# Performance work log

Hardware: AMD Instinct MI355X
Metric: run time of the kernel (lower is better)

## Reference

```python
import jax, jax.numpy as jnp
import numpy as np

B = 16
DRUG_LEN, PROT_LEN = 64, 1200
DIM, CONV = 64, 40


def conv1d(x, w, b):
    # x: [B, C_in, L], w: [C_out, C_in, K] (torch layout), VALID padding
    y = jax.lax.conv_general_dilated(
        x, w, window_strides=(1,), padding='VALID',
        dimension_numbers=('NCH', 'OIH', 'NCH'))
    return y + b[None, :, None]


def setup_inputs() -> dict:
    key = jax.random.key(0)
    ks = jax.random.split(key, 32)
    s = 0.05
    inp = {
        'drug_tokens': jax.random.randint(ks[0], (B, DRUG_LEN), 0, 65, dtype=jnp.int32),
        'protein_tokens': jax.random.randint(ks[1], (B, PROT_LEN), 0, 26, dtype=jnp.int32),
        'drug_emb': (jax.random.normal(ks[2], (65, DIM)) * s).at[0].set(0.0),
        'prot_emb': (jax.random.normal(ks[3], (26, DIM)) * s).at[0].set(0.0),
        'dW1': jax.random.normal(ks[4], (CONV, DIM, 4)) * s,
        'db1': jax.random.normal(ks[5], (CONV,)) * s,
        'dW2': jax.random.normal(ks[6], (CONV * 2, CONV, 6)) * s,
        'db2': jax.random.normal(ks[7], (CONV * 2,)) * s,
        'dW3': jax.random.normal(ks[8], (CONV * 4, CONV * 2, 8)) * s,
        'db3': jax.random.normal(ks[9], (CONV * 4,)) * s,
        'pW1': jax.random.normal(ks[10], (CONV, DIM, 4)) * s,
        'pb1': jax.random.normal(ks[11], (CONV,)) * s,
        'pW2': jax.random.normal(ks[12], (CONV * 2, CONV, 8)) * s,
        'pb2': jax.random.normal(ks[13], (CONV * 2,)) * s,
        'pW3': jax.random.normal(ks[14], (CONV * 4, CONV * 2, 12)) * s,
        'pb3': jax.random.normal(ks[15], (CONV * 4,)) * s,
        'dattW': jax.random.normal(ks[16], (160, 160)) * s,
        'dattb': jax.random.normal(ks[17], (160,)) * s,
        'pattW': jax.random.normal(ks[18], (160, 160)) * s,
        'pattb': jax.random.normal(ks[19], (160,)) * s,
        'attW': jax.random.normal(ks[20], (160, 160)) * s,
        'attb': jax.random.normal(ks[21], (160,)) * s,
        'fc1W': jax.random.normal(ks[22], (1024, 320)) * s,
        'fc1b': jax.random.normal(ks[23], (1024,)) * s,
        'fc2W': jax.random.normal(ks[24], (1024, 1024)) * s,
        'fc2b': jax.random.normal(ks[25], (1024,)) * s,
        'fc3W': jax.random.normal(ks[26], (512, 1024)) * s,
        'fc3b': jax.random.normal(ks[27], (512,)) * s,
        'outW': jax.random.normal(ks[28], (2, 512)) * s,
        'outb': jax.random.normal(ks[29], (2,)) * s,
    }
    return inp


def reference(drug_tokens, protein_tokens, drug_emb, prot_emb,
              dW1, db1, dW2, db2, dW3, db3,
              pW1, pb1, pW2, pb2, pW3, pb3,
              dattW, dattb, pattW, pattb, attW, attb,
              fc1W, fc1b, fc2W, fc2b, fc3W, fc3b, outW, outb):
    relu = jax.nn.relu
    # Embedding lookup, then to [B, C, L]
    de = drug_emb[drug_tokens].transpose(0, 2, 1)    # [B,64,64]
    pe = prot_emb[protein_tokens].transpose(0, 2, 1)  # [B,64,1200]
    # CNN stacks
    dc = relu(conv1d(relu(conv1d(relu(conv1d(de, dW1, db1)), dW2, db2)), dW3, db3))  # [B,160,49]
    pc = relu(conv1d(relu(conv1d(relu(conv1d(pe, pW1, pb1)), pW2, pb2)), pW3, pb3))  # [B,160,1179]
    # Per-token attention projections (Linear over channel dim)
    d_att = jnp.einsum('bcd,oc->bdo', dc, dattW) + dattb   # [B,49,160]
    p_att = jnp.einsum('bcp,oc->bpo', pc, pattW) + pattb   # [B,1179,160]
    # Broadcast outer-sum + ReLU + Linear  -> [B,49,1179,160]
    A = relu(d_att[:, :, None, :] + p_att[:, None, :, :])
    A = jnp.einsum('bdpk,ok->bdpo', A, attW) + attb
    comp_atte = jax.nn.sigmoid(jnp.mean(A, axis=2)).transpose(0, 2, 1)  # [B,160,49]
    prot_atte = jax.nn.sigmoid(jnp.mean(A, axis=1)).transpose(0, 2, 1)  # [B,160,1179]
    dc = dc * 0.5 + dc * comp_atte
    pc = pc * 0.5 + pc * prot_atte
    # Global max pool over length
    dvec = jnp.max(dc, axis=2)  # [B,160]
    pvec = jnp.max(pc, axis=2)  # [B,160]
    pair = jnp.concatenate([dvec, pvec], axis=1)  # [B,320]
    # MLP head (dropout = identity at inference)
    h = jax.nn.leaky_relu(pair @ fc1W.T + fc1b, 0.01)
    h = jax.nn.leaky_relu(h @ fc2W.T + fc2b, 0.01)
    h = jax.nn.leaky_relu(h @ fc3W.T + fc3b, 0.01)
    return h @ outW.T + outb  # [B,2]
```

## Files before the change

### kernel.cpp

```cpp
#include <hip/hip_runtime.h>
#include <hip/hip_bf16.h>

typedef __hip_bfloat16 bf16;
typedef __attribute__((ext_vector_type(8))) short short8;
typedef __attribute__((ext_vector_type(4))) float floatx4;

#define NB 16
#define NPC 48


__device__ __forceinline__ float b2f(bf16 x) { return __bfloat162float(x); }
__device__ __forceinline__ float u16bf(unsigned short u) {
    return __uint_as_float(((unsigned)u) << 16);
}
__device__ __forceinline__ unsigned short f2bu(float v) {
    union { bf16 h; unsigned short u; } cv;
    cv.h = __float2bfloat16(v);
    return cv.u;
}

__global__ void sniff_kernel(const unsigned short* __restrict__ w, int* __restrict__ flag) {
    __shared__ int cnt;
    if (threadIdx.x == 0) cnt = 0;
    __syncthreads();
    int hits = 0;
    for (int s = 0; s < 4; s++) {
        unsigned short u = w[(threadIdx.x * 4 + s) * 2];
        float v = fabsf(u16bf(u));
        if (v > 1e-6f && v < 2.0f) hits++;
    }
    atomicAdd(&cnt, hits);
    __syncthreads();
    if (threadIdx.x == 0) *flag = (cnt > 512) ? 1 : 0;
}

#define NSEG 14
struct CvtJob {
    const void* src[NSEG];
    float* dst[NSEG];
};
#define NPK 11
struct PackJob {
    const void* src[NPK];
    bf16* dst[NPK];
    short Cout[NPK], CIN[NPK], K[NPK], coP[NPK], CIP[NPK];
};
struct PrepOff { int off[NSEG + NPK + 1]; };

__global__ void prep(CvtJob cj, PackJob pj, PrepOff po, const int* __restrict__ flagp) {
    int g = blockIdx.x * 256 + threadIdx.x;
    if (g >= po.off[NSEG + NPK]) return;
    int s = 0;
#pragma unroll
    for (int t = 1; t < NSEG + NPK; t++)
        if (g >= po.off[t]) s = t;
    int i = g - po.off[s];
    if (s < NSEG) {
        const void* sp = cj.src[s];
        if (sp == nullptr) { cj.dst[s][i] = 0.f; return; }
        cj.dst[s][i] = (*flagp) ? b2f(((const bf16*)sp)[i]) : ((const float*)sp)[i];
    } else {
        int p = s - NSEG;
        int Cout = pj.Cout[p], CIN = pj.CIN[p];
        int coP = pj.coP[p], CIP = pj.CIP[p];
        int ci = i % CIP;
        int t = i / CIP;
        int co = t % coP;
        int k = t / coP;
        float v = 0.f;
        if (co < Cout && ci < CIN) {
            int si = (co * CIN + ci) * pj.K[p] + k;
            v = (*flagp) ? b2f(((const bf16*)pj.src[p])[si]) : ((const float*)pj.src[p])[si];
        }
        pj.dst[p][i] = __float2bfloat16(v);
    }
}

template <int K, int CIN, int CHUNKS, int NW>
__device__ __forceinline__ void conv_body(unsigned short* xT,
                                          const unsigned short* xb,
                                          const unsigned short* wbase,
                                          const float* __restrict__ bias,
                                          bf16* __restrict__ y,
                                          int b, int Lin, int Lstride, int Lout,
                                          int Cout, int coP, int l0) {
    const int CIP = CHUNKS * 32;
    const int PCI = CIP + 8;
    const int TLX = 64 + K - 1;
    const int LV = (TLX + 7) >> 3;
    for (int i = threadIdx.x; i < CIP * LV; i += NW * 64) {
        int ci = i / LV, lv = (i - ci * LV) << 3;
        if (ci < CIN && lv + 8 <= TLX && l0 + lv + 8 <= Lin) {
            short8 v = *(const short8*)(xb + ci * Lstride + l0 + lv);
#pragma unroll
            for (int j = 0; j < 8; j++) xT[(lv + j) * PCI + ci] = (unsigned short)v[j];
        } else {
            for (int j = 0; j < 8; j++) {
                int l = lv + j;
                if (l >= TLX) break;
                int gl = l0 + l;
                xT[l * PCI + ci] = (ci < CIN && gl < Lin) ? xb[ci * Lstride + gl]
                                                          : (unsigned short)0;
            }
        }
    }
    __syncthreads();
    int lane = threadIdx.x & 63;
    int ct = threadIdx.x >> 6;
    int n = lane & 15, quad = lane >> 4;
    floatx4 acc[4];
#pragma unroll
    for (int i = 0; i < 4; i++) acc[i] = (floatx4){0.f, 0.f, 0.f, 0.f};
#pragma unroll
    for (int k = 0; k < K; k++) {
#pragma unroll
        for (int ch = 0; ch < CHUNKS; ch++) {
            short8 a = *(const short8*)(wbase +
                        ((size_t)(k * coP + ct * 16 + n)) * CIP + ch * 32 + quad * 8);
#pragma unroll
            for (int nt = 0; nt < 4; nt++) {
                short8 bb = *(const short8*)(xT + (nt * 16 + n + k) * PCI + ch * 32 + quad * 8);
                acc[nt] = __builtin_amdgcn_mfma_f32_16x16x32_bf16(a, bb, acc[nt], 0, 0, 0);
            }
        }
    }
    int m0 = quad * 4;
#pragma unroll
    for (int nt = 0; nt < 4; nt++) {
        int l = l0 + nt * 16 + n;
        if (l >= Lout) continue;
#pragma unroll
        for (int r = 0; r < 4; r++) {
            int co = ct * 16 + m0 + r;
            if (co < Cout)
                y[((size_t)b * Cout + co) * Lout + l] =
                    __float2bfloat16(fmaxf(acc[nt][r] + bias[co], 0.f));
        }
    }
}

template <int KD, int KP, int CIN, int CHUNKS, int NW>
__global__ __launch_bounds__(NW * 64) void conv_dual(const bf16* __restrict__ xd,
                                                 const bf16* __restrict__ Wpd,
                                                 const float* __restrict__ bd,
                                                 bf16* __restrict__ yd,
                                                 int LinD, int LsD, int LoutD,
                                                 const bf16* __restrict__ xp,
                                                 const bf16* __restrict__ Wpp,
                                                 const float* __restrict__ bp,
                                                 bf16* __restrict__ yp,
                                                 int LinP, int LsP, int LoutP,
                                                 int Cout, int coP) {
    const int CIP = CHUNKS * 32;
    const int PCI = CIP + 8;
    const int TLXMAX = 64 + KP - 1;
    __shared__ __align__(16) unsigned short xT[TLXMAX * PCI];
    if (blockIdx.x < 16) {
        int b = blockIdx.x;
        conv_body<KD, CIN, CHUNKS, NW>(xT, (const unsigned short*)xd + (size_t)b * CIN * LsD,
                                   (const unsigned short*)Wpd, bd, yd, b, LinD, LsD, LoutD,
                                   Cout, coP, 0);
    } else {
        int bx = blockIdx.x - 16;
        int b = bx / 19, l0 = (bx % 19) << 6;
        conv_body<KP, CIN, CHUNKS, NW>(xT, (const unsigned short*)xp + (size_t)b * CIN * LsP,
                                   (const unsigned short*)Wpp, bp, yp, b, LinP, LsP, LoutP,
                                   Cout, coP, l0);
    }
}

template <int K, int CIN, int CHUNKS, int NW>
__device__ __forceinline__ void conv_proj_phase(unsigned short* xT, unsigned short* xP,
                                                const unsigned short* xb,
                                                const unsigned short* wbase,
                                                const float* __restrict__ bias,
                                                unsigned short* __restrict__ y,
                                                int b, int Lin, int Lout,
                                                int Cout, int coP, int l0) {
    const int CIP = CHUNKS * 32;
    const int PCI = CIP + 8;
    const int TLX = 64 + K - 1;
    const int LV = (TLX + 7) >> 3;
    for (int i = threadIdx.x; i < CIP * LV; i += NW * 64) {
        int ci = i / LV, lv = (i - ci * LV) << 3;
        if (ci < CIN && lv + 8 <= TLX && l0 + lv + 8 <= Lin) {
            short8 v = *(const short8*)(xb + ci * Lin + l0 + lv);
#pragma unroll
            for (int j = 0; j < 8; j++) xT[(lv + j) * PCI + ci] = (unsigned short)v[j];
        } else {
            for (int j = 0; j < 8; j++) {
                int l = lv + j;
                if (l >= TLX) break;
                int gl = l0 + l;
                xT[l * PCI + ci] = (ci < CIN && gl < Lin) ? xb[ci * Lin + gl]
                                                          : (unsigned short)0;
            }
        }
    }
    __syncthreads();
    int lane = threadIdx.x & 63;
    int ct = threadIdx.x >> 6;
    int n = lane & 15, quad = lane >> 4;
    floatx4 acc[4];
#pragma unroll
    for (int i = 0; i < 4; i++) acc[i] = (floatx4){0.f, 0.f, 0.f, 0.f};
#pragma unroll
    for (int k = 0; k < K; k++) {
#pragma unroll
        for (int ch = 0; ch < CHUNKS; ch++) {
            short8 a = *(const short8*)(wbase +
                        ((size_t)(k * coP + ct * 16 + n)) * CIP + ch * 32 + quad * 8);
#pragma unroll
            for (int nt = 0; nt < 4; nt++) {
                short8 bb = *(const short8*)(xT + (nt * 16 + n + k) * PCI + ch * 32 + quad * 8);
                acc[nt] = __builtin_amdgcn_mfma_f32_16x16x32_bf16(a, bb, acc[nt], 0, 0, 0);
            }
        }
    }
    int m0 = quad * 4;
#pragma unroll
    for (int nt = 0; nt < 4; nt++) {
        int ll = nt * 16 + n;
        int l = l0 + ll;
#pragma unroll
        for (int r = 0; r < 4; r++) {
            int co = ct * 16 + m0 + r;
            float val = (l < Lout) ? fmaxf(acc[nt][r] + bias[co], 0.f) : 0.f;
            unsigned short u = f2bu(val);
            xP[ll * 168 + co] = u;
            if (l < Lout) y[((size_t)b * Cout + co) * Lout + l] = u;
        }
    }
}

template <int KD, int KP, int CIN, int CHUNKS, int NW>
__global__ __launch_bounds__(NW * 64) void conv3_proj(
        const bf16* __restrict__ xd, const bf16* __restrict__ Wpd,
        const float* __restrict__ bd, bf16* __restrict__ yd, int LinD, int LoutD,
        const bf16* __restrict__ xp, const bf16* __restrict__ Wpp,
        const float* __restrict__ bp, bf16* __restrict__ yp, int LinP, int LoutP,
        int Cout, int coP,
        const bf16* __restrict__ dWB, const bf16* __restrict__ pWB,
        const float* __restrict__ dbF, const float* __restrict__ pbF,
        float* __restrict__ datt, bf16* __restrict__ pattB) {
    const int CIP = CHUNKS * 32;
    const int PCI = CIP + 8;
    const int TLXMAX = 64 + KP - 1;
    __shared__ __align__(16) unsigned short xT[TLXMAX * PCI];
    __shared__ __align__(16) unsigned short xP[64 * 168];
    bool isD = blockIdx.x < 16;
    int b, l0, L;
    if (isD) {
        b = blockIdx.x; l0 = 0; L = LoutD;
        conv_proj_phase<KD, CIN, CHUNKS, NW>(xT, xP,
            (const unsigned short*)xd + (size_t)b * CIN * LinD,
            (const unsigned short*)Wpd, bd, (unsigned short*)yd, b, LinD, LoutD, Cout, coP, 0);
    } else {
        int bx = blockIdx.x - 16;
        b = bx / 19; l0 = (bx % 19) << 6; L = LoutP;
        conv_proj_phase<KP, CIN, CHUNKS, NW>(xT, xP,
            (const unsigned short*)xp + (size_t)b * CIN * LinP,
            (const unsigned short*)Wpp, bp, (unsigned short*)yp, b, LinP, LoutP, Cout, coP, l0);
    }
    __syncthreads();
    int lane = threadIdx.x & 63;
    int t = threadIdx.x >> 6;
    int n = lane & 15, quad = lane >> 4;
    const unsigned short* W = (const unsigned short*)(isD ? dWB : pWB);
    const float* pbias = isD ? dbF : pbF;
    floatx4 acc[4];
#pragma unroll
    for (int i = 0; i < 4; i++) acc[i] = (floatx4){0.f, 0.f, 0.f, 0.f};
#pragma unroll
    for (int ch = 0; ch < 5; ch++) {
        short8 a = *(const short8*)(W + ((size_t)(t * 16 + n)) * 160 + ch * 32 + quad * 8);
#pragma unroll
        for (int nt = 0; nt < 4; nt++) {
            short8 bb = *(const short8*)(xP + (nt * 16 + n) * 168 + ch * 32 + quad * 8);
            acc[nt] = __builtin_amdgcn_mfma_f32_16x16x32_bf16(a, bb, acc[nt], 0, 0, 0);
        }
    }
    int m0 = quad * 4;
    int o0 = t * 16 + m0;
#pragma unroll
    for (int nt = 0; nt < 4; nt++) {
        int l = l0 + nt * 16 + n;
        if (l >= L) continue;
        if (isD) {
            float4 v;
            v.x = acc[nt][0] + pbias[o0 + 0];
            v.y = acc[nt][1] + pbias[o0 + 1];
            v.z = acc[nt][2] + pbias[o0 + 2];
            v.w = acc[nt][3] + pbias[o0 + 3];
            *(float4*)(datt + ((size_t)b * 49 + l) * 160 + o0) = v;
        } else {
            ushort4 u;
            u.x = f2bu(acc[nt][0] + pbias[o0 + 0]);
            u.y = f2bu(acc[nt][1] + pbias[o0 + 1]);
            u.z = f2bu(acc[nt][2] + pbias[o0 + 2]);
            u.w = f2bu(acc[nt][3] + pbias[o0 + 3]);
            *(ushort4*)((unsigned short*)pattB + ((size_t)b * 1179 + l) * 160 + o0) = u;
        }
    }
}

__global__ __launch_bounds__(256) void conv1_mfma(const int* __restrict__ dtok,
                                                  const int* __restrict__ ptok,
                                                  const bf16* __restrict__ embDB,
                                                  const bf16* __restrict__ embPB,
                                                  const bf16* __restrict__ dW1p,
                                                  const bf16* __restrict__ pW1p,
                                                  const float* __restrict__ db1f,
                                                  const float* __restrict__ pb1f,
                                                  bf16* __restrict__ d1,
                                                  bf16* __restrict__ p1) {
    const int K = 4, CIP = 64, PCI = 72, TLX = 67, coP = 48, Cout = 40;
    __shared__ __align__(16) unsigned short xT[TLX * PCI];
    __shared__ int stok[TLX];
    bool isD = blockIdx.x < 16;
    int b, l0, Lin, Lout, Ostride;
    const int* tok; const unsigned short* embB; const unsigned short* Wp;
    const float* bias; bf16* y;
    if (isD) {
        b = blockIdx.x; l0 = 0; Lin = 64; Lout = 61; Ostride = 62;
        tok = dtok; embB = (const unsigned short*)embDB;
        Wp = (const unsigned short*)dW1p; bias = db1f; y = d1;
    } else {
        int bx = blockIdx.x - 16;
        b = bx / 19; l0 = (bx % 19) << 6; Lin = 1200; Lout = 1197; Ostride = 1198;
        tok = ptok; embB = (const unsigned short*)embPB;
        Wp = (const unsigned short*)pW1p; bias = pb1f; y = p1;
    }
    if (threadIdx.x < TLX) {
        int l = l0 + threadIdx.x;
        stok[threadIdx.x] = (l < Lin) ? tok[b * Lin + l] : -1;
    }
    __syncthreads();
    for (int i = threadIdx.x; i < TLX * 8; i += 256) {
        int l = i >> 3, c8 = (i & 7) << 3;
        int t = stok[l];
        short8 v = (short8){0, 0, 0, 0, 0, 0, 0, 0};
        if (t >= 0) v = *(const short8*)(embB + t * 64 + c8);
        *(short8*)(xT + l * PCI + c8) = v;
    }
    __syncthreads();
    int lane = threadIdx.x & 63;
    int w = threadIdx.x >> 6;
    int n = lane & 15, quad = lane >> 4;
    if (w >= 3) return;
    floatx4 acc[4];
#pragma unroll
    for (int i = 0; i < 4; i++) acc[i] = (floatx4){0.f, 0.f, 0.f, 0.f};
#pragma unroll
    for (int k = 0; k < K; k++) {
#pragma unroll
        for (int ch = 0; ch < 2; ch++) {
            short8 a = *(const short8*)(Wp +
                        ((size_t)(k * coP + w * 16 + n)) * CIP + ch * 32 + quad * 8);
#pragma unroll
            for (int nt = 0; nt < 4; nt++) {
                short8 bb = *(const short8*)(xT + (nt * 16 + n + k) * PCI + ch * 32 + quad * 8);
                acc[nt] = __builtin_amdgcn_mfma_f32_16x16x32_bf16(a, bb, acc[nt], 0, 0, 0);
            }
        }
    }
    int m0 = quad * 4;
#pragma unroll
    for (int nt = 0; nt < 4; nt++) {
        int l = l0 + nt * 16 + n;
        if (l >= Lout) continue;
#pragma unroll
        for (int r = 0; r < 4; r++) {
            int co = w * 16 + m0 + r;
            if (co < Cout)
                y[((size_t)b * Cout + co) * Ostride + l] =
                    __float2bfloat16(fmaxf(acc[nt][r] + bias[co], 0.f));
        }
    }
}

__global__ __launch_bounds__(640) void mean_fused(const float* __restrict__ datt,
                                                  const bf16* __restrict__ patt,
                                                  bf16* __restrict__ MpW,
                                                  float* __restrict__ Mdpart) {
    __shared__ __align__(16) unsigned short sp[25 * 160];
    int tid = threadIdx.x;
    int b = blockIdx.x / NPC;
    int pc = blockIdx.x % NPC;
    int p0 = pc * 25;
    int pmax = 1179 - p0;
    if (pmax > 25) pmax = 25;
    {
        const short8* src = (const short8*)((const unsigned short*)patt +
                                            ((size_t)b * 1179 + p0) * 160);
        short8* dst = (short8*)sp;
        int n8 = (pmax * 160) >> 3;
        for (int v = tid; v < n8; v += 640) dst[v] = src[v];
    }
    int h = tid & 3;
    int k = tid >> 2;
    int d0 = h * 13;
    int nd = (h == 3) ? 10 : 13;
    const float* drow = datt + (size_t)b * 49 * 160 + k;
    float dv[13], md[13];
#pragma unroll
    for (int i = 0; i < 13; i++) {
        dv[i] = (i < nd) ? drow[(d0 + i) * 160] : -1e30f;
        md[i] = 0.f;
    }
    __syncthreads();
    unsigned short* mp = (unsigned short*)MpW + ((size_t)b * 1184 + p0) * 160 + k;
#pragma unroll 2
    for (int pi = 0; pi < pmax; pi++) {
        float pv = u16bf(sp[pi * 160 + k]);
        float s0 = 0.f, s1 = 0.f, s2 = 0.f, s3 = 0.f;
#pragma unroll
        for (int g = 0; g < 3; g++) {
            float r0 = fmaxf(dv[g * 4 + 0] + pv, 0.f);
            float r1 = fmaxf(dv[g * 4 + 1] + pv, 0.f);
            float r2 = fmaxf(dv[g * 4 + 2] + pv, 0.f);
            float r3 = fmaxf(dv[g * 4 + 3] + pv, 0.f);
            md[g * 4 + 0] += r0; s0 += r0;
            md[g * 4 + 1] += r1; s1 += r1;
            md[g * 4 + 2] += r2; s2 += r2;
            md[g * 4 + 3] += r3; s3 += r3;
        }
        {
            float r = fmaxf(dv[12] + pv, 0.f);
            md[12] += r; s0 += r;
        }
        float s = (s0 + s1) + (s2 + s3);
        s += __shfl_xor(s, 1, 64);
        s += __shfl_xor(s, 2, 64);
        if (h == 0) mp[(size_t)pi * 160] = f2bu(s * (1.f / 49.f));
    }
    float* op = Mdpart + (((size_t)b * NPC + pc) * 49) * 160 + k;
#pragma unroll
    for (int i = 0; i < 13; i++)
        if (i < nd) op[(d0 + i) * 160] = md[i];
}

__global__ __launch_bounds__(256) void md_reduce(const float* __restrict__ Mdpart,
                                                 float* __restrict__ Md) {
    int i = blockIdx.x * 256 + threadIdx.x;
    if (i >= NB * 49 * 160) return;
    int b = i / (49 * 160);
    int dk = i - b * (49 * 160);
    const float* src = Mdpart + (size_t)b * NPC * 7840 + dk;
    float s0 = 0.f, s1 = 0.f, s2 = 0.f, s3 = 0.f;
#pragma unroll
    for (int pc = 0; pc < NPC; pc += 4) {
        s0 += src[(size_t)(pc + 0) * 7840];
        s1 += src[(size_t)(pc + 1) * 7840];
        s2 += src[(size_t)(pc + 2) * 7840];
        s3 += src[(size_t)(pc + 3) * 7840];
    }
    Md[i] = (s0 + s1) + (s2 + s3);
}

__global__ __launch_bounds__(640) void att_sig_mfma(const float* __restrict__ Md,
                                                    const bf16* __restrict__ MpW,
                                                    const bf16* __restrict__ wattB,
                                                    const float* __restrict__ attbF,
                                                    const bf16* __restrict__ dcB,
                                                    const bf16* __restrict__ pcB,
                                                    float* __restrict__ pair) {
    const int PCI = 168;
    __shared__ __align__(16) unsigned short sM[64 * PCI];
    bool isD = blockIdx.x < 16;
    int b, p0, L, off;
    const unsigned short* conv;
    if (isD) {
        b = blockIdx.x; p0 = 0; L = 49; off = 0; conv = (const unsigned short*)dcB;
        for (int i = threadIdx.x; i < 160 * 64; i += 640) {
            int r = i / 160, k = i - r * 160;
            float v = (r < 49) ? Md[((size_t)b * 49 + r) * 160 + k] * (1.f / 1179.f) : 0.f;
            sM[r * PCI + k] = f2bu(v);
        }
    } else {
        int bx = blockIdx.x - 16;
        b = bx / 19; p0 = (bx % 19) << 6; L = 1179; off = 160;
        conv = (const unsigned short*)pcB;
        const unsigned short* mb = (const unsigned short*)MpW + (size_t)b * 1184 * 160;
        for (int i = threadIdx.x; i < 64 * 20; i += 640) {
            int r = i / 20, k8 = (i - r * 20) << 3;
            int p = p0 + r;
            short8 v = (short8){0, 0, 0, 0, 0, 0, 0, 0};
            if (p < 1179) v = *(const short8*)(mb + (size_t)p * 160 + k8);
            *(short8*)(sM + r * PCI + k8) = v;
        }
    }
    __syncthreads();
    int lane = threadIdx.x & 63;
    int t = threadIdx.x >> 6;
    int n = lane & 15, quad = lane >> 4;
    floatx4 acc[4];
#pragma unroll
    for (int i = 0; i < 4; i++) acc[i] = (floatx4){0.f, 0.f, 0.f, 0.f};
    const unsigned short* W = (const unsigned short*)wattB;
#pragma unroll
    for (int ch = 0; ch < 5; ch++) {
        short8 a = *(const short8*)(W + ((size_t)(t * 16 + n)) * 160 + ch * 32 + quad * 8);
#pragma unroll
        for (int nt = 0; nt < 4; nt++) {
            short8 bb = *(const short8*)(sM + (nt * 16 + n) * PCI + ch * 32 + quad * 8);
            acc[nt] = __builtin_amdgcn_mfma_f32_16x16x32_bf16(a, bb, acc[nt], 0, 0, 0);
        }
    }
    int m0 = quad * 4;
    float vmax[4] = {0.f, 0.f, 0.f, 0.f};
#pragma unroll
    for (int nt = 0; nt < 4; nt++) {
        int p = p0 + nt * 16 + n;
#pragma unroll
        for (int r = 0; r < 4; r++) {
            int o = t * 16 + m0 + r;
            float sig = 1.f / (1.f + __expf(-(acc[nt][r] + attbF[o])));
            float v = 0.f;
            if (p < L) v = u16bf(conv[((size_t)b * 160 + o) * L + p]) * (0.5f + sig);
            vmax[r] = fmaxf(vmax[r], v);
        }
    }
#pragma unroll
    for (int m = 1; m < 16; m <<= 1) {
#pragma unroll
        for (int r = 0; r < 4; r++)
            vmax[r] = fmaxf(vmax[r], __shfl_xor(vmax[r], m, 64));
    }
    if (n == 0) {
#pragma unroll
        for (int r = 0; r < 4; r++)
            atomicMax((unsigned int*)(pair + b * 320 + off + t * 16 + m0 + r),
                      __float_as_uint(vmax[r]));
    }
}

__global__ __launch_bounds__(256) void fc_block(const float* __restrict__ in,
                                                const void* __restrict__ W,
                                                const float* __restrict__ bias,
                                                float* __restrict__ out,
                                                int IN, int OUT,
                                                const int* __restrict__ flagp) {
    int j = blockIdx.x;
    int w = threadIdx.x >> 6, li = threadIdx.x & 63;
    int nv = IN >> 2;
    const float4* i0 = (const float4*)(in + (size_t)(w * 4 + 0) * IN);
    const float4* i1 = (const float4*)(in + (size_t)(w * 4 + 1) * IN);
    const float4* i2 = (const float4*)(in + (size_t)(w * 4 + 2) * IN);
    const float4* i3 = (const float4*)(in + (size_t)(w * 4 + 3) * IN);
    float p0 = 0.f, p1 = 0.f, p2 = 0.f, p3 = 0.f;
    if (*flagp) {
        const ushort4* w4 = (const ushort4*)((const unsigned short*)W + (size_t)j * IN);
        for (int v = li; v < nv; v += 64) {
            ushort4 u = w4[v];
            float wa = u16bf(u.x), wb = u16bf(u.y), wc = u16bf(u.z), wd = u16bf(u.w);
            float4 x;
            x = i0[v]; p0 += x.x * wa + x.y * wb + x.z * wc + x.w * wd;
            x = i1[v]; p1 += x.x * wa + x.y * wb + x.z * wc + x.w * wd;
            x = i2[v]; p2 += x.x * wa + x.y * wb + x.z * wc + x.w * wd;
            x = i3[v]; p3 += x.x * wa + x.y * wb + x.z * wc + x.w * wd;
        }
    } else {
        const float4* w4 = (const float4*)((const float*)W + (size_t)j * IN);
        for (int v = li; v < nv; v += 64) {
            float4 u = w4[v];
            float4 x;
            x = i0[v]; p0 += x.x * u.x + x.y * u.y + x.z * u.z + x.w * u.w;
            x = i1[v]; p1 += x.x * u.x + x.y * u.y + x.z * u.z + x.w * u.w;
            x = i2[v]; p2 += x.x * u.x + x.y * u.y + x.z * u.z + x.w * u.w;
            x = i3[v]; p3 += x.x * u.x + x.y * u.y + x.z * u.z + x.w * u.w;
        }
    }
#pragma unroll
    for (int m = 1; m < 64; m <<= 1) {
        p0 += __shfl_xor(p0, m, 64);
        p1 += __shfl_xor(p1, m, 64);
        p2 += __shfl_xor(p2, m, 64);
        p3 += __shfl_xor(p3, m, 64);
    }
    if (li == 0) {
        float bj = bias[j];
        float o0 = p0 + bj, o1 = p1 + bj, o2 = p2 + bj, o3 = p3 + bj;
        o0 = o0 > 0.f ? o0 : 0.01f * o0;
        o1 = o1 > 0.f ? o1 : 0.01f * o1;
        o2 = o2 > 0.f ? o2 : 0.01f * o2;
        o3 = o3 > 0.f ? o3 : 0.01f * o3;
        out[(size_t)(w * 4 + 0) * OUT + j] = o0;
        out[(size_t)(w * 4 + 1) * OUT + j] = o1;
        out[(size_t)(w * 4 + 2) * OUT + j] = o2;
        out[(size_t)(w * 4 + 3) * OUT + j] = o3;
    }
}

__global__ __launch_bounds__(256) void out_block(const float* __restrict__ h,
                                                 const void* __restrict__ W,
                                                 const float* __restrict__ biasF,
                                                 void* __restrict__ out,
                                                 const int* __restrict__ flagp) {
    int j = blockIdx.x;
    int w = threadIdx.x >> 6, li = threadIdx.x & 63;
    const int IN = 512, nv = 128;
    const float4* i0 = (const float4*)(h + (size_t)(w * 4 + 0) * IN);
    const float4* i1 = (const float4*)(h + (size_t)(w * 4 + 1) * IN);
    const float4* i2 = (const float4*)(h + (size_t)(w * 4 + 2) * IN);
    const float4* i3 = (const float4*)(h + (size_t)(w * 4 + 3) * IN);
    float p0 = 0.f, p1 = 0.f, p2 = 0.f, p3 = 0.f;
    int flag = *flagp;
    if (flag) {
        const ushort4* w4 = (const ushort4*)((const unsigned short*)W + (size_t)j * IN);
        for (int v = li; v < nv; v += 64) {
            ushort4 u = w4[v];
            float wa = u16bf(u.x), wb = u16bf(u.y), wc = u16bf(u.z), wd = u16bf(u.w);
            float4 x;
            x = i0[v]; p0 += x.x * wa + x.y * wb + x.z * wc + x.w * wd;
            x = i1[v]; p1 += x.x * wa + x.y * wb + x.z * wc + x.w * wd;
            x = i2[v]; p2 += x.x * wa + x.y * wb + x.z * wc + x.w * wd;
            x = i3[v]; p3 += x.x * wa + x.y * wb + x.z * wc + x.w * wd;
        }
    } else {
        const float4* w4 = (const float4*)((const float*)W + (size_t)j * IN);
        for (int v = li; v < nv; v += 64) {
            float4 u = w4[v];
            float4 x;
            x = i0[v]; p0 += x.x * u.x + x.y * u.y + x.z * u.z + x.w * u.w;
            x = i1[v]; p1 += x.x * u.x + x.y * u.y + x.z * u.z + x.w * u.w;
            x = i2[v]; p2 += x.x * u.x + x.y * u.y + x.z * u.z + x.w * u.w;
            x = i3[v]; p3 += x.x * u.x + x.y * u.y + x.z * u.z + x.w * u.w;
        }
    }
#pragma unroll
    for (int m = 1; m < 64; m <<= 1) {
        p0 += __shfl_xor(p0, m, 64);
        p1 += __shfl_xor(p1, m, 64);
        p2 += __shfl_xor(p2, m, 64);
        p3 += __shfl_xor(p3, m, 64);
    }
    if (li == 0) {
        float bj = biasF[j];
        float o0 = p0 + bj, o1 = p1 + bj, o2 = p2 + bj, o3 = p3 + bj;
        if (flag) {
            bf16* ob = (bf16*)out;
            ob[(w * 4 + 0) * 2 + j] = __float2bfloat16(o0);
            ob[(w * 4 + 1) * 2 + j] = __float2bfloat16(o1);
            ob[(w * 4 + 2) * 2 + j] = __float2bfloat16(o2);
            ob[(w * 4 + 3) * 2 + j] = __float2bfloat16(o3);
        } else {
            float* of = (float*)out;
            of[(w * 4 + 0) * 2 + j] = o0;
            of[(w * 4 + 1) * 2 + j] = o1;
            of[(w * 4 + 2) * 2 + j] = o2;
            of[(w * 4 + 3) * 2 + j] = o3;
        }
    }
}

extern "C" void kernel_launch(void* const* d_in, const int* in_sizes, int n_in,
                              void* d_out, int out_size, void* d_ws, size_t ws_size,
                              hipStream_t stream) {
    const int* drug_tok = (const int*)d_in[0];
    const int* prot_tok = (const int*)d_in[1];
    const void* drug_emb = d_in[2];
    const void* prot_emb = d_in[3];
    const void* dW1 = d_in[4];  const void* db1 = d_in[5];
    const void* dW2 = d_in[6];  const void* db2 = d_in[7];
    const void* dW3 = d_in[8];  const void* db3 = d_in[9];
    const void* pW1 = d_in[10]; const void* pb1 = d_in[11];
    const void* pW2 = d_in[12]; const void* pb2 = d_in[13];
    const void* pW3 = d_in[14]; const void* pb3 = d_in[15];
    const void* dattW = d_in[16]; const void* dattb = d_in[17];
    const void* pattW = d_in[18]; const void* pattb = d_in[19];
    const void* attW  = d_in[20]; const void* attb  = d_in[21];
    const void* fc1W = d_in[22]; const void* fc1b = d_in[23];
    const void* fc2W = d_in[24]; const void* fc2b = d_in[25];
    const void* fc3W = d_in[26]; const void* fc3b = d_in[27];
    const void* outW = d_in[28]; const void* outb = d_in[29];

    char* base = (char*)d_ws;
    size_t cur = 0;
    auto alloc = [&](size_t bytes) -> char* {
        char* p = base + cur;
        cur = (cur + bytes + 255) & ~(size_t)255;
        return p;
    };
    int*   flag  = (int*)alloc(256);
    bf16* embDB = (bf16*)alloc(65 * 64 * 2);
    bf16* embPB = (bf16*)alloc(26 * 64 * 2);
    bf16* dW1p = (bf16*)alloc((size_t)4 * 48 * 64 * 2);
    bf16* pW1p = (bf16*)alloc((size_t)4 * 48 * 64 * 2);
    bf16* dW2p = (bf16*)alloc((size_t)6 * 128 * 64 * 2);
    bf16* dW3p = (bf16*)alloc((size_t)8 * 192 * 96 * 2);
    bf16* pW2p = (bf16*)alloc((size_t)8 * 128 * 64 * 2);
    bf16* pW3p = (bf16*)alloc((size_t)12 * 192 * 96 * 2);
    float* db1f = (float*)alloc(40 * 4);
    float* db2f = (float*)alloc(80 * 4);
    float* db3f = (float*)alloc(160 * 4);
    float* pb1f = (float*)alloc(40 * 4);
    float* pb2f = (float*)alloc(80 * 4);
    float* pb3f = (float*)alloc(160 * 4);
    float* dattbF = (float*)alloc(160 * 4);
    float* pattbF = (float*)alloc(160 * 4);
    float* attbF  = (float*)alloc(160 * 4);
    float* fc1bF = (float*)alloc(1024 * 4);
    float* fc2bF = (float*)alloc(1024 * 4);
    float* fc3bF = (float*)alloc(512 * 4);
    float* outbF = (float*)alloc(2 * 4);
    bf16* dattWB = (bf16*)alloc(25600 * 2);
    bf16* pattWB = (bf16*)alloc(25600 * 2);
    bf16* wattB  = (bf16*)alloc(25600 * 2);
    bf16* d1  = (bf16*)alloc((size_t)NB * 40 * 62 * 2);
    bf16* d2  = (bf16*)alloc((size_t)NB * 80 * 56 * 2);
    bf16* dcB = (bf16*)alloc((size_t)NB * 160 * 49 * 2);
    bf16* p1  = (bf16*)alloc((size_t)NB * 40 * 1198 * 2);
    bf16* p2  = (bf16*)alloc((size_t)NB * 80 * 1190 * 2);
    bf16* pcB = (bf16*)alloc((size_t)NB * 160 * 1179 * 2);
    float* datt  = (float*)alloc((size_t)NB * 49 * 160 * 4);
    bf16* pattB = (bf16*)alloc((size_t)NB * 1179 * 160 * 2);
    float* Md   = (float*)alloc((size_t)NB * 49 * 160 * 4);
    float* Mdpart = (float*)alloc((size_t)NB * NPC * 49 * 160 * 4);
    bf16* MpW  = (bf16*)alloc((size_t)NB * 1184 * 160 * 2);
    float* pair = (float*)alloc(NB * 320 * 4);
    float* h1 = (float*)alloc(NB * 1024 * 4);
    float* h2 = (float*)alloc(NB * 1024 * 4);
    float* h3 = (float*)alloc(NB * 512 * 4);

    sniff_kernel<<<1, 256, 0, stream>>>((const unsigned short*)fc2W, flag);

    CvtJob cj;
    PackJob pj;
    PrepOff po;
    int si = 0, running = 0;
    auto add = [&](const void* s, float* d, int n) {
        cj.src[si] = s; cj.dst[si] = d; po.off[si] = running; running += n; si++;
    };
    add(db1, db1f, 40); add(db2, db2f, 80); add(db3, db3f, 160);
    add(pb1, pb1f, 40); add(pb2, pb2f, 80); add(pb3, pb3f, 160);
    add(dattb, dattbF, 160); add(pattb, pattbF, 160); add(attb, attbF, 160);
    add(fc1b, fc1bF, 1024); add(fc2b, fc2bF, 1024); add(fc3b, fc3bF, 512);
    add(outb, outbF, 2);
    add(nullptr, pair, NB * 320);
    int pi = 0;
    auto seg = [&](const void* s, bf16* d, int Cout, int CIN, int K, int coP, int CIP) {
        pj.src[pi] = s; pj.dst[pi] = d;
        pj.Cout[pi] = Cout; pj.CIN[pi] = CIN; pj.K[pi] = K; pj.coP[pi] = coP; pj.CIP[pi] = CIP;
        po.off[NSEG + pi] = running; running += K * coP * CIP; pi++;
    };
    seg(dW1, dW1p, 40, 64, 4, 48, 64);
    seg(pW1, pW1p, 40, 64, 4, 48, 64);
    seg(dW2, dW2p, 80, 40, 6, 128, 64);
    seg(pW2, pW2p, 80, 40, 8, 128, 64);
    seg(dW3, dW3p, 160, 80, 8, 192, 96);
    seg(pW3, pW3p, 160, 80, 12, 192, 96);
    seg(dattW, dattWB, 160, 160, 1, 160, 160);
    seg(pattW, pattWB, 160, 160, 1, 160, 160);
    seg(attW,  wattB,  160, 160, 1, 160, 160);
    seg(drug_emb, embDB, 65, 64, 1, 65, 64);
    seg(prot_emb, embPB, 26, 64, 1, 26, 64);
    po.off[NSEG + NPK] = running;
    prep<<<(running + 255) / 256, 256, 0, stream>>>(cj, pj, po, flag);

    conv1_mfma<<<16 + 16 * 19, 256, 0, stream>>>(drug_tok, prot_tok, embDB, embPB,
                                                 dW1p, pW1p, db1f, pb1f, d1, p1);
    conv_dual<6, 8, 40, 2, 5><<<320, 320, 0, stream>>>(
        d1, dW2p, db2f, d2, 61, 62, 56,
        p1, pW2p, pb2f, p2, 1197, 1198, 1190, 80, 128);
    conv3_proj<8, 12, 80, 3, 10><<<320, 640, 0, stream>>>(
        d2, dW3p, db3f, dcB, 56, 49,
        p2, pW3p, pb3f, pcB, 1190, 1179, 160, 192,
        dattWB, pattWB, dattbF, pattbF, datt, pattB);

    mean_fused<<<16 * NPC, 640, 0, stream>>>(datt, pattB, MpW, Mdpart);
    md_reduce<<<490, 256, 0, stream>>>(Mdpart, Md);

    att_sig_mfma<<<320, 640, 0, stream>>>(Md, MpW, wattB, attbF, dcB, pcB, pair);

    fc_block<<<1024, 256, 0, stream>>>(pair, fc1W, fc1bF, h1, 320, 1024, flag);
    fc_block<<<1024, 256, 0, stream>>>(h1, fc2W, fc2bF, h2, 1024, 1024, flag);
    fc_block<<<512, 256, 0, stream>>>(h2, fc3W, fc3bF, h3, 1024, 512, flag);
    out_block<<<2, 256, 0, stream>>>(h3, outW, outbF, d_out, flag);
}
```

Before: 223.9 us.

## Fuse MLP head into one per-sample kernel and fold dtype sniff into prep

The four separate fully-connected launches are replaced by a single kernel with one 1024-thread block per batch row. Each block keeps its activations in shared memory and each thread computes one output neuron by walking a full weight row. The separate sniff kernel that guesses the weight dtype is merged into the prep kernel, where every block recomputes the flag locally. This removes several launches and the global round trips for the intermediate activations. In exchange only 16 blocks run, each thread reads a strided weight row with poor coalescing, and every block re-reads all weights from L2.

```diff
diff --git a/kernel.cpp b/kernel.cpp
--- a/kernel.cpp
+++ b/kernel.cpp
@@ -17,21 +17,6 @@
     union { bf16 h; unsigned short u; } cv;
     cv.h = __float2bfloat16(v);
     return cv.u;
-}
-
-__global__ void sniff_kernel(const unsigned short* __restrict__ w, int* __restrict__ flag) {
-    __shared__ int cnt;
-    if (threadIdx.x == 0) cnt = 0;
-    __syncthreads();
-    int hits = 0;
-    for (int s = 0; s < 4; s++) {
-        unsigned short u = w[(threadIdx.x * 4 + s) * 2];
-        float v = fabsf(u16bf(u));
-        if (v > 1e-6f && v < 2.0f) hits++;
-    }
-    atomicAdd(&cnt, hits);
-    __syncthreads();
-    if (threadIdx.x == 0) *flag = (cnt > 512) ? 1 : 0;
 }
 
 #define NSEG 14
@@ -47,7 +32,21 @@
 };
 struct PrepOff { int off[NSEG + NPK + 1]; };
 
-__global__ void prep(CvtJob cj, PackJob pj, PrepOff po, const int* __restrict__ flagp) {
+__global__ void prep(CvtJob cj, PackJob pj, PrepOff po,
+                     const unsigned short* __restrict__ sniffw, int* __restrict__ flagg) {
+    __shared__ int cnt;
+    if (threadIdx.x == 0) cnt = 0;
+    __syncthreads();
+    int hits = 0;
+    for (int s = 0; s < 4; s++) {
+        unsigned short u = sniffw[(threadIdx.x * 4 + s) * 2];
+        float v = fabsf(u16bf(u));
+        if (v > 1e-6f && v < 2.0f) hits++;
+    }
+    atomicAdd(&cnt, hits);
+    __syncthreads();
+    int flag = (cnt > 512) ? 1 : 0;
+    if (threadIdx.x == 0 && blockIdx.x == 0) *flagg = flag;
     int g = blockIdx.x * 256 + threadIdx.x;
     if (g >= po.off[NSEG + NPK]) return;
     int s = 0;
@@ -58,7 +57,7 @@
     if (s < NSEG) {
         const void* sp = cj.src[s];
         if (sp == nullptr) { cj.dst[s][i] = 0.f; return; }
-        cj.dst[s][i] = (*flagp) ? b2f(((const bf16*)sp)[i]) : ((const float*)sp)[i];
+        cj.dst[s][i] = flag ? b2f(((const bf16*)sp)[i]) : ((const float*)sp)[i];
     } else {
         int p = s - NSEG;
         int Cout = pj.Cout[p], CIN = pj.CIN[p];
@@ -70,7 +69,7 @@
         float v = 0.f;
         if (co < Cout && ci < CIN) {
             int si = (co * CIN + ci) * pj.K[p] + k;
-            v = (*flagp) ? b2f(((const bf16*)pj.src[p])[si]) : ((const float*)pj.src[p])[si];
+            v = flag ? b2f(((const bf16*)pj.src[p])[si]) : ((const float*)pj.src[p])[si];
         }
         pj.dst[p][i] = __float2bfloat16(v);
     }
@@ -535,121 +534,108 @@
     }
 }
 
-__global__ __launch_bounds__(256) void fc_block(const float* __restrict__ in,
-                                                const void* __restrict__ W,
-                                                const float* __restrict__ bias,
-                                                float* __restrict__ out,
-                                                int IN, int OUT,
-                                                const int* __restrict__ flagp) {
-    int j = blockIdx.x;
-    int w = threadIdx.x >> 6, li = threadIdx.x & 63;
-    int nv = IN >> 2;
-    const float4* i0 = (const float4*)(in + (size_t)(w * 4 + 0) * IN);
-    const float4* i1 = (const float4*)(in + (size_t)(w * 4 + 1) * IN);
-    const float4* i2 = (const float4*)(in + (size_t)(w * 4 + 2) * IN);
-    const float4* i3 = (const float4*)(in + (size_t)(w * 4 + 3) * IN);
-    float p0 = 0.f, p1 = 0.f, p2 = 0.f, p3 = 0.f;
-    if (*flagp) {
-        const ushort4* w4 = (const ushort4*)((const unsigned short*)W + (size_t)j * IN);
-        for (int v = li; v < nv; v += 64) {
-            ushort4 u = w4[v];
-            float wa = u16bf(u.x), wb = u16bf(u.y), wc = u16bf(u.z), wd = u16bf(u.w);
-            float4 x;
-            x = i0[v]; p0 += x.x * wa + x.y * wb + x.z * wc + x.w * wd;
-            x = i1[v]; p1 += x.x * wa + x.y * wb + x.z * wc + x.w * wd;
-            x = i2[v]; p2 += x.x * wa + x.y * wb + x.z * wc + x.w * wd;
-            x = i3[v]; p3 += x.x * wa + x.y * wb + x.z * wc + x.w * wd;
-        }
-    } else {
-        const float4* w4 = (const float4*)((const float*)W + (size_t)j * IN);
-        for (int v = li; v < nv; v += 64) {
-            float4 u = w4[v];
-            float4 x;
-            x = i0[v]; p0 += x.x * u.x + x.y * u.y + x.z * u.z + x.w * u.w;
-            x = i1[v]; p1 += x.x * u.x + x.y * u.y + x.z * u.z + x.w * u.w;
-            x = i2[v]; p2 += x.x * u.x + x.y * u.y + x.z * u.z + x.w * u.w;
-            x = i3[v]; p3 += x.x * u.x + x.y * u.y + x.z * u.z + x.w * u.w;
-        }
-    }
-#pragma unroll
-    for (int m = 1; m < 64; m <<= 1) {
-        p0 += __shfl_xor(p0, m, 64);
-        p1 += __shfl_xor(p1, m, 64);
-        p2 += __shfl_xor(p2, m, 64);
-        p3 += __shfl_xor(p3, m, 64);
-    }
-    if (li == 0) {
-        float bj = bias[j];
-        float o0 = p0 + bj, o1 = p1 + bj, o2 = p2 + bj, o3 = p3 + bj;
-        o0 = o0 > 0.f ? o0 : 0.01f * o0;
-        o1 = o1 > 0.f ? o1 : 0.01f * o1;
-        o2 = o2 > 0.f ? o2 : 0.01f * o2;
-        o3 = o3 > 0.f ? o3 : 0.01f * o3;
-        out[(size_t)(w * 4 + 0) * OUT + j] = o0;
-        out[(size_t)(w * 4 + 1) * OUT + j] = o1;
-        out[(size_t)(w * 4 + 2) * OUT + j] = o2;
-        out[(size_t)(w * 4 + 3) * OUT + j] = o3;
-    }
-}
-
-__global__ __launch_bounds__(256) void out_block(const float* __restrict__ h,
-                                                 const void* __restrict__ W,
-                                                 const float* __restrict__ biasF,
-                                                 void* __restrict__ out,
-                                                 const int* __restrict__ flagp) {
-    int j = blockIdx.x;
-    int w = threadIdx.x >> 6, li = threadIdx.x & 63;
-    const int IN = 512, nv = 128;
-    const float4* i0 = (const float4*)(h + (size_t)(w * 4 + 0) * IN);
-    const float4* i1 = (const float4*)(h + (size_t)(w * 4 + 1) * IN);
-    const float4* i2 = (const float4*)(h + (size_t)(w * 4 + 2) * IN);
-    const float4* i3 = (const float4*)(h + (size_t)(w * 4 + 3) * IN);
-    float p0 = 0.f, p1 = 0.f, p2 = 0.f, p3 = 0.f;
+__global__ __launch_bounds__(1024) void mlp_all(const float* __restrict__ pair,
+        const void* __restrict__ W1, const float* __restrict__ b1,
+        const void* __restrict__ W2, const float* __restrict__ b2,
+        const void* __restrict__ W3, const float* __restrict__ b3,
+        const void* __restrict__ W4, const float* __restrict__ b4f,
+        void* __restrict__ dout, const int* __restrict__ flagp) {
+    __shared__ __align__(16) float xa[1024];
+    __shared__ __align__(16) float xb[1024];
+    int b = blockIdx.x, t = threadIdx.x;
     int flag = *flagp;
-    if (flag) {
-        const ushort4* w4 = (const ushort4*)((const unsigned short*)W + (size_t)j * IN);
-        for (int v = li; v < nv; v += 64) {
-            ushort4 u = w4[v];
-            float wa = u16bf(u.x), wb = u16bf(u.y), wc = u16bf(u.z), wd = u16bf(u.w);
-            float4 x;
-            x = i0[v]; p0 += x.x * wa + x.y * wb + x.z * wc + x.w * wd;
-            x = i1[v]; p1 += x.x * wa + x.y * wb + x.z * wc + x.w * wd;
-            x = i2[v]; p2 += x.x * wa + x.y * wb + x.z * wc + x.w * wd;
-            x = i3[v]; p3 += x.x * wa + x.y * wb + x.z * wc + x.w * wd;
-        }
-    } else {
-        const float4* w4 = (const float4*)((const float*)W + (size_t)j * IN);
-        for (int v = li; v < nv; v += 64) {
-            float4 u = w4[v];
-            float4 x;
-            x = i0[v]; p0 += x.x * u.x + x.y * u.y + x.z * u.z + x.w * u.w;
-            x = i1[v]; p1 += x.x * u.x + x.y * u.y + x.z * u.z + x.w * u.w;
-            x = i2[v]; p2 += x.x * u.x + x.y * u.y + x.z * u.z + x.w * u.w;
-            x = i3[v]; p3 += x.x * u.x + x.y * u.y + x.z * u.z + x.w * u.w;
-        }
-    }
-#pragma unroll
-    for (int m = 1; m < 64; m <<= 1) {
-        p0 += __shfl_xor(p0, m, 64);
-        p1 += __shfl_xor(p1, m, 64);
-        p2 += __shfl_xor(p2, m, 64);
-        p3 += __shfl_xor(p3, m, 64);
-    }
-    if (li == 0) {
-        float bj = biasF[j];
-        float o0 = p0 + bj, o1 = p1 + bj, o2 = p2 + bj, o3 = p3 + bj;
+    if (t < 320) xa[t] = pair[b * 320 + t];
+    __syncthreads();
+    {
+        float acc = 0.f;
+        const float4* xs = (const float4*)xa;
         if (flag) {
-            bf16* ob = (bf16*)out;
-            ob[(w * 4 + 0) * 2 + j] = __float2bfloat16(o0);
-            ob[(w * 4 + 1) * 2 + j] = __float2bfloat16(o1);
-            ob[(w * 4 + 2) * 2 + j] = __float2bfloat16(o2);
-            ob[(w * 4 + 3) * 2 + j] = __float2bfloat16(o3);
+            const ushort4* w = (const ushort4*)((const unsigned short*)W1 + (size_t)t * 320);
+#pragma unroll 4
+            for (int v = 0; v < 80; v++) {
+                ushort4 u = w[v]; float4 x = xs[v];
+                acc += x.x * u16bf(u.x) + x.y * u16bf(u.y) + x.z * u16bf(u.z) + x.w * u16bf(u.w);
+            }
         } else {
-            float* of = (float*)out;
-            of[(w * 4 + 0) * 2 + j] = o0;
-            of[(w * 4 + 1) * 2 + j] = o1;
-            of[(w * 4 + 2) * 2 + j] = o2;
-            of[(w * 4 + 3) * 2 + j] = o3;
+            const float4* w = (const float4*)((const float*)W1 + (size_t)t * 320);
+#pragma unroll 4
+            for (int v = 0; v < 80; v++) {
+                float4 u = w[v]; float4 x = xs[v];
+                acc += x.x * u.x + x.y * u.y + x.z * u.z + x.w * u.w;
+            }
+        }
+        acc += b1[t];
+        xb[t] = acc > 0.f ? acc : 0.01f * acc;
+    }
+    __syncthreads();
+    {
+        float acc = 0.f;
+        const float4* xs = (const float4*)xb;
+        if (flag) {
+            const ushort4* w = (const ushort4*)((const unsigned short*)W2 + (size_t)t * 1024);
+#pragma unroll 4
+            for (int v = 0; v < 256; v++) {
+                ushort4 u = w[v]; float4 x = xs[v];
+                acc += x.x * u16bf(u.x) + x.y * u16bf(u.y) + x.z * u16bf(u.z) + x.w * u16bf(u.w);
+            }
+        } else {
+            const float4* w = (const float4*)((const float*)W2 + (size_t)t * 1024);
+#pragma unroll 4
+            for (int v = 0; v < 256; v++) {
+                float4 u = w[v]; float4 x = xs[v];
+                acc += x.x * u.x + x.y * u.y + x.z * u.z + x.w * u.w;
+            }
+        }
+        acc += b2[t];
+        xa[t] = acc > 0.f ? acc : 0.01f * acc;
+    }
+    __syncthreads();
+    if (t < 512) {
+        float acc = 0.f;
+        const float4* xs = (const float4*)xa;
+        if (flag) {
+            const ushort4* w = (const ushort4*)((const unsigned short*)W3 + (size_t)t * 1024);
+#pragma unroll 4
+            for (int v = 0; v < 256; v++) {
+                ushort4 u = w[v]; float4 x = xs[v];
+                acc += x.x * u16bf(u.x) + x.y * u16bf(u.y) + x.z * u16bf(u.z) + x.w * u16bf(u.w);
+            }
+        } else {
+            const float4* w = (const float4*)((const float*)W3 + (size_t)t * 1024);
+#pragma unroll 4
+            for (int v = 0; v < 256; v++) {
+                float4 u = w[v]; float4 x = xs[v];
+                acc += x.x * u.x + x.y * u.y + x.z * u.z + x.w * u.w;
+            }
+        }
+        acc += b3[t];
+        xb[t] = acc > 0.f ? acc : 0.01f * acc;
+    }
+    __syncthreads();
+    if (t < 128) {
+        int j = t >> 6, lane = t & 63;
+        float acc = 0.f;
+        if (flag) {
+            const unsigned short* w = (const unsigned short*)W4 + (size_t)j * 512;
+#pragma unroll
+            for (int k = 0; k < 8; k++) {
+                int i = lane + k * 64;
+                acc += xb[i] * u16bf(w[i]);
+            }
+        } else {
+            const float* w = (const float*)W4 + (size_t)j * 512;
+#pragma unroll
+            for (int k = 0; k < 8; k++) {
+                int i = lane + k * 64;
+                acc += xb[i] * w[i];
+            }
+        }
+#pragma unroll
+        for (int m = 1; m < 64; m <<= 1) acc += __shfl_xor(acc, m, 64);
+        if (lane == 0) {
+            float o = acc + b4f[j];
+            if (flag) ((bf16*)dout)[b * 2 + j] = __float2bfloat16(o);
+            else      ((float*)dout)[b * 2 + j] = o;
         }
     }
 }
@@ -719,11 +705,6 @@
     float* Mdpart = (float*)alloc((size_t)NB * NPC * 49 * 160 * 4);
     bf16* MpW  = (bf16*)alloc((size_t)NB * 1184 * 160 * 2);
     float* pair = (float*)alloc(NB * 320 * 4);
-    float* h1 = (float*)alloc(NB * 1024 * 4);
-    float* h2 = (float*)alloc(NB * 1024 * 4);
-    float* h3 = (float*)alloc(NB * 512 * 4);
-
-    sniff_kernel<<<1, 256, 0, stream>>>((const unsigned short*)fc2W, flag);
 
     CvtJob cj;
     PackJob pj;
@@ -756,7 +737,8 @@
     seg(drug_emb, embDB, 65, 64, 1, 65, 64);
     seg(prot_emb, embPB, 26, 64, 1, 26, 64);
     po.off[NSEG + NPK] = running;
-    prep<<<(running + 255) / 256, 256, 0, stream>>>(cj, pj, po, flag);
+    prep<<<(running + 255) / 256, 256, 0, stream>>>(cj, pj, po,
+                                                    (const unsigned short*)fc2W, flag);
 
     conv1_mfma<<<16 + 16 * 19, 256, 0, stream>>>(drug_tok, prot_tok, embDB, embPB,
                                                  dW1p, pW1p, db1f, pb1f, d1, p1);
@@ -773,8 +755,6 @@
 
     att_sig_mfma<<<320, 640, 0, stream>>>(Md, MpW, wattB, attbF, dcB, pcB, pair);
 
-    fc_block<<<1024, 256, 0, stream>>>(pair, fc1W, fc1bF, h1, 320, 1024, flag);
-    fc_block<<<1024, 256, 0, stream>>>(h1, fc2W, fc2bF, h2, 1024, 1024, flag);
-    fc_block<<<512, 256, 0, stream>>>(h2, fc3W, fc3bF, h3, 1024, 512, flag);
-    out_block<<<2, 256, 0, stream>>>(h3, outW, outbF, d_out, flag);
-}
+    mlp_all<<<16, 1024, 0, stream>>>(pair, fc1W, fc1bF, fc2W, fc2bF,
+                                     fc3W, fc3bF, outW, outbF, d_out, flag);
+}
```

Result: slower. 423.5 us (+89.1%).
